# Kernel tuning notes

Hardware: AMD Instinct MI355X
Metric: run time of the kernel (lower is better)

## Reference

```python
import jax, jax.numpy as jnp
import numpy as np

HIDDEN = 32  # hard-coded in the module


def _lstm_cell(x, h, c, W_ih, W_hh, b_ih, b_hh):
    # torch.nn.LSTMCell: gates in order i, f, g, o
    gates = x @ W_ih.T + b_ih + h @ W_hh.T + b_hh
    i, f, g, o = jnp.split(gates, 4, axis=-1)
    c_new = jax.nn.sigmoid(f) * c + jax.nn.sigmoid(i) * jnp.tanh(g)
    h_new = jax.nn.sigmoid(o) * jnp.tanh(c_new)
    return h_new, c_new


def setup_inputs() -> dict:
    key = jax.random.key(0)
    ks = jax.random.split(key, 11)
    B, T, d, len_out = 256, 1024, 8, 10
    s = 0.05
    return {
        "input": jax.random.normal(ks[0], (B, T, d), dtype=jnp.float32),
        "W_ih1": jax.random.normal(ks[1], (4 * HIDDEN, d), dtype=jnp.float32) * s,
        "W_hh1": jax.random.normal(ks[2], (4 * HIDDEN, HIDDEN), dtype=jnp.float32) * s,
        "b_ih1": jax.random.normal(ks[3], (4 * HIDDEN,), dtype=jnp.float32) * s,
        "b_hh1": jax.random.normal(ks[4], (4 * HIDDEN,), dtype=jnp.float32) * s,
        "W_ih2": jax.random.normal(ks[5], (4 * HIDDEN, HIDDEN), dtype=jnp.float32) * s,
        "W_hh2": jax.random.normal(ks[6], (4 * HIDDEN, HIDDEN), dtype=jnp.float32) * s,
        "b_ih2": jax.random.normal(ks[7], (4 * HIDDEN,), dtype=jnp.float32) * s,
        "b_hh2": jax.random.normal(ks[8], (4 * HIDDEN,), dtype=jnp.float32) * s,
        "W_lin": jax.random.normal(ks[9], (d * len_out, HIDDEN), dtype=jnp.float32) * s,
        "b_lin": jax.random.normal(ks[10], (d * len_out,), dtype=jnp.float32) * s,
    }


def reference(input, W_ih1, W_hh1, b_ih1, b_hh1, W_ih2, W_hh2, b_ih2, b_hh2, W_lin, b_lin):
    B, T, d = input.shape
    len_out = W_lin.shape[0] // d

    def step(carry, x_t):
        h1, c1, h2, c2 = carry
        h1, c1 = _lstm_cell(x_t, h1, c1, W_ih1, W_hh1, b_ih1, b_hh1)
        h2, c2 = _lstm_cell(h1, h2, c2, W_ih2, W_hh2, b_ih2, b_hh2)
        out = h2 @ W_lin.T + b_lin  # [B, d*len_out]
        return (h1, c1, h2, c2), out

    z = jnp.zeros((B, HIDDEN), dtype=input.dtype)
    init = (z, z, z, z)
    xs = jnp.swapaxes(input, 0, 1)  # [T, B, d]
    _, outs = jax.lax.scan(step, init, xs)  # [T, B, d*len_out]
    outs = jnp.swapaxes(outs, 0, 1)  # [B, T, d*len_out]
    return outs.reshape(B, T, d, len_out)
```

## Files before the change

kernel.cpp:

```cpp
#include <hip/hip_runtime.h>

#define TT  1024
#define DIN 8

__device__ __forceinline__ float fsig(float x) {
    float e = __builtin_amdgcn_exp2f(-1.4426950408889634f * x);
    return __builtin_amdgcn_rcpf(1.0f + e);
}
__device__ __forceinline__ float ftanh_(float x) {
    float e = __builtin_amdgcn_exp2f(-2.8853900817779268f * x);
    return 2.0f * __builtin_amdgcn_rcpf(1.0f + e) - 1.0f;
}
template<int CTRL>
__device__ __forceinline__ float dppf(float v) {
    return __uint_as_float((unsigned)__builtin_amdgcn_update_dpp(
        0, (int)__float_as_uint(v), CTRL, 0xF, 0xF, true));
}
#define RED8(a)  { a += dppf<0x141>(a); a += dppf<0x1B>(a); a += dppf<0xB1>(a); }

__device__ __forceinline__ void bar_lgkm() {
    asm volatile("s_waitcnt lgkmcnt(0)\n\ts_barrier" ::: "memory");
}

__global__ void __launch_bounds__(512, 2)
lstm_rec(const float* __restrict__ x,
         const float* __restrict__ Wih1, const float* __restrict__ Whh1,
         const float* __restrict__ bih1, const float* __restrict__ bhh1,
         const float* __restrict__ Wih2, const float* __restrict__ Whh2,
         const float* __restrict__ bih2, const float* __restrict__ bhh2,
         float* __restrict__ out)
{
    const int tid = threadIdx.x;
    const int wv  = tid >> 6;
    const int l   = tid & 63;
    const int s   = l & 7;
    const int gi  = l >> 3;
    const int b   = blockIdx.x;
    const bool isL1 = (wv < 4);
    const int  wu   = isL1 ? wv : (wv - 4);
    const int  unit = wu*8 + gi;

    __shared__ float hb1[2][32];
    __shared__ float hb2[2][32];
    if (tid < 64)       ((float*)hb1)[tid]      = 0.f;
    else if (tid < 128) ((float*)hb2)[tid - 64] = 0.f;

    float w[32];
    float bi, bf, bg, bo;
    if (isL1) {
#pragma unroll
        for (int r = 0; r < 4; ++r) {
            const int R = r*32 + unit;
#pragma unroll
            for (int j = 0; j < 4; ++j) w[r*4 + j] = Whh1[R*32 + s*4 + j];
            w[16 + r] = Wih1[R*DIN + s];
        }
        bi = bih1[unit]      + bhh1[unit];
        bf = bih1[32 + unit] + bhh1[32 + unit];
        bg = bih1[64 + unit] + bhh1[64 + unit];
        bo = bih1[96 + unit] + bhh1[96 + unit];
    } else {
        const float* Wb = (s < 4) ? Whh2 : Wih2;
        const int co = (s & 3) * 8;
#pragma unroll
        for (int r = 0; r < 4; ++r) {
            const int R = r*32 + unit;
#pragma unroll
            for (int j = 0; j < 8; ++j) w[r*8 + j] = Wb[R*32 + co + j];
        }
        bi = bih2[unit]      + bhh2[unit];
        bf = bih2[32 + unit] + bhh2[32 + unit];
        bg = bih2[64 + unit] + bhh2[64 + unit];
        bo = bih2[96 + unit] + bhh2[96 + unit];
    }

    float c = 0.f;

    const float* __restrict__ xb = x   + (size_t)b * (TT*DIN);
    float* __restrict__ outb     = out + (size_t)b * (TT*80);

    float xcur = 0.f;
    if (isL1) xcur = xb[s];
    int xoff = DIN + s;
    const int XMAX = (TT-1)*DIN + s;
    int o2 = 0;

    bar_lgkm();

#pragma unroll 1
    for (int t = 0; t <= TT; ++t) {
        const int p0  = t & 1;
        const int pm1 = p0 ^ 1;

        if (isL1) {
            if (t < TT) {
                float4 h4 = *reinterpret_cast<const float4*>(&hb1[pm1][s*4]);
                float ai = w[0] *h4.x + w[16]*xcur;
                float af = w[4] *h4.x + w[17]*xcur;
                float ag = w[8] *h4.x + w[18]*xcur;
                float ao = w[12]*h4.x + w[19]*xcur;
                ai += w[1]*h4.y;  af += w[5]*h4.y;  ag += w[9] *h4.y;  ao += w[13]*h4.y;
                ai += w[2]*h4.z;  af += w[6]*h4.z;  ag += w[10]*h4.z;  ao += w[14]*h4.z;
                ai += w[3]*h4.w;  af += w[7]*h4.w;  ag += w[11]*h4.w;  ao += w[15]*h4.w;
                xcur = xb[xoff];
                xoff = (xoff + DIN > XMAX) ? XMAX : (xoff + DIN);
                RED8(ai); RED8(af); RED8(ag); RED8(ao);
                float si = fsig(ai + bi);
                float sf = fsig(af + bf);
                float tg = ftanh_(ag + bg);
                float so = fsig(ao + bo);
                c = sf * c + si * tg;
                float hv = so * ftanh_(c);
                if (s == 0) hb1[p0][unit] = hv;
            }
        } else {
            if (t >= 1) {
                const float* hin = (s < 4) ? &hb2[p0][(s & 3) * 8]
                                           : &hb1[pm1][(s & 3) * 8];
                float4 u0 = reinterpret_cast<const float4*>(hin)[0];
                float4 u1 = reinterpret_cast<const float4*>(hin)[1];
                float ai = w[0] *u0.x, af = w[8] *u0.x, ag = w[16]*u0.x, ao = w[24]*u0.x;
                ai += w[1]*u0.y;  af += w[9] *u0.y;  ag += w[17]*u0.y;  ao += w[25]*u0.y;
                ai += w[2]*u0.z;  af += w[10]*u0.z;  ag += w[18]*u0.z;  ao += w[26]*u0.z;
                ai += w[3]*u0.w;  af += w[11]*u0.w;  ag += w[19]*u0.w;  ao += w[27]*u0.w;
                ai += w[4]*u1.x;  af += w[12]*u1.x;  ag += w[20]*u1.x;  ao += w[28]*u1.x;
                ai += w[5]*u1.y;  af += w[13]*u1.y;  ag += w[21]*u1.y;  ao += w[29]*u1.y;
                ai += w[6]*u1.z;  af += w[14]*u1.z;  ag += w[22]*u1.z;  ao += w[30]*u1.z;
                ai += w[7]*u1.w;  af += w[15]*u1.w;  ag += w[23]*u1.w;  ao += w[31]*u1.w;
                RED8(ai); RED8(af); RED8(ag); RED8(ao);
                float si = fsig(ai + bi);
                float sf = fsig(af + bf);
                float tg = ftanh_(ag + bg);
                float so = fsig(ao + bo);
                c = sf * c + si * tg;
                float hv = so * ftanh_(c);
                if (s == 0) {
                    hb2[pm1][unit] = hv;
                    outb[o2 + unit] = hv;
                }
                o2 += 80;
            }
        }

        bar_lgkm();
    }
}

__global__ void __launch_bounds__(256, 4)
out_lin(const float* __restrict__ Wlin, const float* __restrict__ blin,
        float* __restrict__ out, int ntiles)
{
    __shared__ float wl[80][36];
    __shared__ float bl[80];
    __shared__ float ht[16][36];
    const int tid = threadIdx.x;

#pragma unroll 1
    for (int i = tid; i < 640; i += 256) {
        const int cc = i >> 3, qq = i & 7;
        float4 v = reinterpret_cast<const float4*>(Wlin)[i];
        *reinterpret_cast<float4*>(&wl[cc][qq*4]) = v;
    }
    if (tid < 80) bl[tid] = blin[tid];
    __syncthreads();

    const int row = tid >> 4;
    const int cl  = tid & 15;

#pragma unroll 1
    for (int tile = blockIdx.x; tile < ntiles; tile += gridDim.x) {
        const size_t base = (size_t)tile * 16;
        if (tid < 128) {
            const int r = tid >> 3, qq = tid & 7;
            float4 v = *reinterpret_cast<const float4*>(out + (base + r)*80 + qq*4);
            *reinterpret_cast<float4*>(&ht[r][qq*4]) = v;
        }
        __syncthreads();

        float hr[32];
#pragma unroll
        for (int j = 0; j < 8; ++j) {
            float4 v = *reinterpret_cast<const float4*>(&ht[row][j*4]);
            hr[4*j]=v.x; hr[4*j+1]=v.y; hr[4*j+2]=v.z; hr[4*j+3]=v.w;
        }
        float res[5];
#pragma unroll
        for (int cj = 0; cj < 5; ++cj) {
            const int cc = cl + 16*cj;
            float a0 = bl[cc], a1 = 0.f, a2 = 0.f, a3 = 0.f;
#pragma unroll
            for (int k = 0; k < 32; k += 4) {
                a0 += wl[cc][k]  *hr[k];   a1 += wl[cc][k+1]*hr[k+1];
                a2 += wl[cc][k+2]*hr[k+2]; a3 += wl[cc][k+3]*hr[k+3];
            }
            res[cj] = (a0 + a1) + (a2 + a3);
        }
        __syncthreads();
#pragma unroll
        for (int cj = 0; cj < 5; ++cj)
            out[(base + row)*80 + cl + 16*cj] = res[cj];
    }
}

extern "C" void kernel_launch(void* const* d_in, const int* in_sizes, int n_in,
                              void* d_out, int out_size, void* d_ws, size_t ws_size,
                              hipStream_t stream) {
    const float* x    = (const float*)d_in[0];
    const float* Wih1 = (const float*)d_in[1];
    const float* Whh1 = (const float*)d_in[2];
    const float* bih1 = (const float*)d_in[3];
    const float* bhh1 = (const float*)d_in[4];
    const float* Wih2 = (const float*)d_in[5];
    const float* Whh2 = (const float*)d_in[6];
    const float* bih2 = (const float*)d_in[7];
    const float* bhh2 = (const float*)d_in[8];
    const float* Wlin = (const float*)d_in[9];
    const float* blin = (const float*)d_in[10];

    const int B = in_sizes[0] / (TT * DIN);
    const int ntiles = (B * TT) / 16;

    hipLaunchKernelGGL(lstm_rec, dim3(B), dim3(512), 0, stream,
                       x, Wih1, Whh1, bih1, bhh1,
                       Wih2, Whh2, bih2, bhh2,
                       (float*)d_out);
    hipLaunchKernelGGL(out_lin, dim3(2048), dim3(256), 0, stream,
                       Wlin, blin, (float*)d_out, ntiles);
}
```

Measured before the change: 425.0 us.

## Split LSTM gates across lanes with 1024-thread blocks and DPP gate exchange

Doubles the recurrent block to 1024 threads so each lane group of 4 computes one gate row instead of 8 lanes computing all four gates. This cuts the per-step dot-product chain, reduction depth and transcendental count per lane: one sigmoid per lane, with tanh for the g gate folded into it. Gate values are then exchanged through row DPP shuffles. In exchange the block barrier now spans 16 waves, and occupancy or register limits change with the new launch bounds.

```diff
diff --git a/kernel.cpp b/kernel.cpp
--- a/kernel.cpp
+++ b/kernel.cpp
@@ -16,13 +16,13 @@
     return __uint_as_float((unsigned)__builtin_amdgcn_update_dpp(
         0, (int)__float_as_uint(v), CTRL, 0xF, 0xF, true));
 }
-#define RED8(a)  { a += dppf<0x141>(a); a += dppf<0x1B>(a); a += dppf<0xB1>(a); }
+#define RED4(a)  { a += dppf<0x1B>(a); a += dppf<0xB1>(a); }
 
 __device__ __forceinline__ void bar_lgkm() {
     asm volatile("s_waitcnt lgkmcnt(0)\n\ts_barrier" ::: "memory");
 }
 
-__global__ void __launch_bounds__(512, 2)
+__global__ void __launch_bounds__(1024, 4)
 lstm_rec(const float* __restrict__ x,
          const float* __restrict__ Wih1, const float* __restrict__ Whh1,
          const float* __restrict__ bih1, const float* __restrict__ bhh1,
@@ -30,48 +30,39 @@
          const float* __restrict__ bih2, const float* __restrict__ bhh2,
          float* __restrict__ out)
 {
-    const int tid = threadIdx.x;
-    const int wv  = tid >> 6;
-    const int l   = tid & 63;
-    const int s   = l & 7;
-    const int gi  = l >> 3;
-    const int b   = blockIdx.x;
-    const bool isL1 = (wv < 4);
-    const int  wu   = isL1 ? wv : (wv - 4);
-    const int  unit = wu*8 + gi;
+    const int tid  = threadIdx.x;
+    const int wv   = tid >> 6;
+    const int l    = tid & 63;
+    const int sl   = l & 3;
+    const int gate = (l >> 2) & 3;
+    const int ul   = l >> 4;
+    const int b    = blockIdx.x;
+    const bool isL1 = (wv < 8);
+    const int  wu   = isL1 ? wv : (wv - 8);
+    const int  unit = wu*4 + ul;
+    const int  R    = gate*32 + unit;
+    const bool isg  = (gate == 2);
 
     __shared__ float hb1[2][32];
     __shared__ float hb2[2][32];
     if (tid < 64)       ((float*)hb1)[tid]      = 0.f;
     else if (tid < 128) ((float*)hb2)[tid - 64] = 0.f;
 
-    float w[32];
-    float bi, bf, bg, bo;
+    float wh[16];
+    float wx0 = 0.f, wx1 = 0.f;
+    float bias;
     if (isL1) {
 #pragma unroll
-        for (int r = 0; r < 4; ++r) {
-            const int R = r*32 + unit;
-#pragma unroll
-            for (int j = 0; j < 4; ++j) w[r*4 + j] = Whh1[R*32 + s*4 + j];
-            w[16 + r] = Wih1[R*DIN + s];
-        }
-        bi = bih1[unit]      + bhh1[unit];
-        bf = bih1[32 + unit] + bhh1[32 + unit];
-        bg = bih1[64 + unit] + bhh1[64 + unit];
-        bo = bih1[96 + unit] + bhh1[96 + unit];
+        for (int j = 0; j < 8; ++j) wh[j] = Whh1[R*32 + sl*8 + j];
+        wx0 = Wih1[R*DIN + sl*2];
+        wx1 = Wih1[R*DIN + sl*2 + 1];
+        bias = bih1[R] + bhh1[R];
     } else {
-        const float* Wb = (s < 4) ? Whh2 : Wih2;
-        const int co = (s & 3) * 8;
-#pragma unroll
-        for (int r = 0; r < 4; ++r) {
-            const int R = r*32 + unit;
-#pragma unroll
-            for (int j = 0; j < 8; ++j) w[r*8 + j] = Wb[R*32 + co + j];
-        }
-        bi = bih2[unit]      + bhh2[unit];
-        bf = bih2[32 + unit] + bhh2[32 + unit];
-        bg = bih2[64 + unit] + bhh2[64 + unit];
-        bo = bih2[96 + unit] + bhh2[96 + unit];
+        const float* Wb = (sl < 2) ? (Whh2 + R*32 + sl*16)
+                                   : (Wih2 + R*32 + (sl-2)*16);
+#pragma unroll
+        for (int j = 0; j < 16; ++j) wh[j] = Wb[j];
+        bias = bih2[R] + bhh2[R];
     }
 
     float c = 0.f;
@@ -79,10 +70,10 @@
     const float* __restrict__ xb = x   + (size_t)b * (TT*DIN);
     float* __restrict__ outb     = out + (size_t)b * (TT*80);
 
-    float xcur = 0.f;
-    if (isL1) xcur = xb[s];
-    int xoff = DIN + s;
-    const int XMAX = (TT-1)*DIN + s;
+    float2 xcur = make_float2(0.f, 0.f);
+    if (isL1) xcur = *reinterpret_cast<const float2*>(xb + sl*2);
+    int xoff = DIN + sl*2;
+    const int XMAX = (TT-1)*DIN + sl*2;
     int o2 = 0;
 
     bar_lgkm();
@@ -94,47 +85,60 @@
 
         if (isL1) {
             if (t < TT) {
-                float4 h4 = *reinterpret_cast<const float4*>(&hb1[pm1][s*4]);
-                float ai = w[0] *h4.x + w[16]*xcur;
-                float af = w[4] *h4.x + w[17]*xcur;
-                float ag = w[8] *h4.x + w[18]*xcur;
-                float ao = w[12]*h4.x + w[19]*xcur;
-                ai += w[1]*h4.y;  af += w[5]*h4.y;  ag += w[9] *h4.y;  ao += w[13]*h4.y;
-                ai += w[2]*h4.z;  af += w[6]*h4.z;  ag += w[10]*h4.z;  ao += w[14]*h4.z;
-                ai += w[3]*h4.w;  af += w[7]*h4.w;  ag += w[11]*h4.w;  ao += w[15]*h4.w;
-                xcur = xb[xoff];
+                const float* hin = &hb1[pm1][sl*8];
+                float4 u0 = reinterpret_cast<const float4*>(hin)[0];
+                float4 u1 = reinterpret_cast<const float4*>(hin)[1];
+                float a0 = wh[0]*u0.x + wx0*xcur.x;
+                float a1 = wh[1]*u0.y + wx1*xcur.y;
+                float a2 = wh[2]*u0.z;
+                float a3 = wh[3]*u0.w;
+                a0 += wh[4]*u1.x;  a1 += wh[5]*u1.y;
+                a2 += wh[6]*u1.z;  a3 += wh[7]*u1.w;
+                xcur = *reinterpret_cast<const float2*>(xb + xoff);
                 xoff = (xoff + DIN > XMAX) ? XMAX : (xoff + DIN);
-                RED8(ai); RED8(af); RED8(ag); RED8(ao);
-                float si = fsig(ai + bi);
-                float sf = fsig(af + bf);
-                float tg = ftanh_(ag + bg);
-                float so = fsig(ao + bo);
-                c = sf * c + si * tg;
+
+                float acc = (a0 + a1) + (a2 + a3);
+                RED4(acc);
+                float full = acc + bias;
+                float u  = isg ? (full + full) : full;
+                float S  = fsig(u);
+                float av = isg ? (S + S - 1.0f) : S;
+                float si = dppf<0x118>(av);
+                float sf = dppf<0x114>(av);
+                float so = dppf<0x104>(av);
+                c = sf * c + si * av;
                 float hv = so * ftanh_(c);
-                if (s == 0) hb1[p0][unit] = hv;
+                if ((l & 15) == 8) hb1[p0][unit] = hv;
             }
         } else {
             if (t >= 1) {
-                const float* hin = (s < 4) ? &hb2[p0][(s & 3) * 8]
-                                           : &hb1[pm1][(s & 3) * 8];
+                const float* hin = (sl < 2) ? &hb2[p0][sl*16]
+                                            : &hb1[pm1][(sl-2)*16];
                 float4 u0 = reinterpret_cast<const float4*>(hin)[0];
                 float4 u1 = reinterpret_cast<const float4*>(hin)[1];
-                float ai = w[0] *u0.x, af = w[8] *u0.x, ag = w[16]*u0.x, ao = w[24]*u0.x;
-                ai += w[1]*u0.y;  af += w[9] *u0.y;  ag += w[17]*u0.y;  ao += w[25]*u0.y;
-                ai += w[2]*u0.z;  af += w[10]*u0.z;  ag += w[18]*u0.z;  ao += w[26]*u0.z;
-                ai += w[3]*u0.w;  af += w[11]*u0.w;  ag += w[19]*u0.w;  ao += w[27]*u0.w;
-                ai += w[4]*u1.x;  af += w[12]*u1.x;  ag += w[20]*u1.x;  ao += w[28]*u1.x;
-                ai += w[5]*u1.y;  af += w[13]*u1.y;  ag += w[21]*u1.y;  ao += w[29]*u1.y;
-                ai += w[6]*u1.z;  af += w[14]*u1.z;  ag += w[22]*u1.z;  ao += w[30]*u1.z;
-                ai += w[7]*u1.w;  af += w[15]*u1.w;  ag += w[23]*u1.w;  ao += w[31]*u1.w;
-                RED8(ai); RED8(af); RED8(ag); RED8(ao);
-                float si = fsig(ai + bi);
-                float sf = fsig(af + bf);
-                float tg = ftanh_(ag + bg);
-                float so = fsig(ao + bo);
-                c = sf * c + si * tg;
+                float4 u2 = reinterpret_cast<const float4*>(hin)[2];
+                float4 u3 = reinterpret_cast<const float4*>(hin)[3];
+                float a0 = wh[0] *u0.x, a1 = wh[1] *u0.y;
+                float a2 = wh[2] *u0.z, a3 = wh[3] *u0.w;
+                a0 += wh[4] *u1.x;  a1 += wh[5] *u1.y;
+                a2 += wh[6] *u1.z;  a3 += wh[7] *u1.w;
+                a0 += wh[8] *u2.x;  a1 += wh[9] *u2.y;
+                a2 += wh[10]*u2.z;  a3 += wh[11]*u2.w;
+                a0 += wh[12]*u3.x;  a1 += wh[13]*u3.y;
+                a2 += wh[14]*u3.z;  a3 += wh[15]*u3.w;
+
+                float acc = (a0 + a1) + (a2 + a3);
+                RED4(acc);
+                float full = acc + bias;
+                float u  = isg ? (full + full) : full;
+                float S  = fsig(u);
+                float av = isg ? (S + S - 1.0f) : S;
+                float si = dppf<0x118>(av);
+                float sf = dppf<0x114>(av);
+                float so = dppf<0x104>(av);
+                c = sf * c + si * av;
                 float hv = so * ftanh_(c);
-                if (s == 0) {
+                if ((l & 15) == 8) {
                     hb2[pm1][unit] = hv;
                     outb[o2 + unit] = hv;
                 }
@@ -220,7 +224,7 @@
     const int B = in_sizes[0] / (TT * DIN);
     const int ntiles = (B * TT) / 16;
 
-    hipLaunchKernelGGL(lstm_rec, dim3(B), dim3(512), 0, stream,
+    hipLaunchKernelGGL(lstm_rec, dim3(B), dim3(1024), 0, stream,
                        x, Wih1, Whh1, bih1, bhh1,
                        Wih2, Whh2, bih2, bhh2,
                        (float*)d_out);
```

Measured after the change: 461.1 us. 8.5% more time.

## Decouple LSTM layers into producer/consumer waves with LDS ring and flags

Applied to the files above, without the earlier changes.

Replaces the 512-thread block with per-timestep barriers by two single-wave roles: wave 0 runs layer 1 and writes h1 into a 256-entry LDS ring, and wave 1 runs layer 2 and consumes the ring. The two waves coordinate through spin-waited progress counters in shared memory instead of block barriers. Each lane pair owns one hidden unit with full-row weights in registers, so packed FMAs and a single DPP swap replace the 8-lane reduction. This removes per-step barrier latency and lets layer 1 run ahead of layer 2. In exchange each wave does more serial work per step, and ordering depends on volatile LDS flags with sleep-based polling.

```diff
diff --git a/kernel.cpp b/kernel.cpp
--- a/kernel.cpp
+++ b/kernel.cpp
@@ -1,7 +1,10 @@
 #include <hip/hip_runtime.h>
 
-#define TT  1024
-#define DIN 8
+#define TT   1024
+#define DIN  8
+#define RING 256
+
+typedef float f32x2 __attribute__((ext_vector_type(2)));
 
 __device__ __forceinline__ float fsig(float x) {
     float e = __builtin_amdgcn_exp2f(-1.4426950408889634f * x);
@@ -16,13 +19,11 @@
     return __uint_as_float((unsigned)__builtin_amdgcn_update_dpp(
         0, (int)__float_as_uint(v), CTRL, 0xF, 0xF, true));
 }
-#define RED8(a)  { a += dppf<0x141>(a); a += dppf<0x1B>(a); a += dppf<0xB1>(a); }
-
-__device__ __forceinline__ void bar_lgkm() {
-    asm volatile("s_waitcnt lgkmcnt(0)\n\ts_barrier" ::: "memory");
-}
-
-__global__ void __launch_bounds__(512, 2)
+__device__ __forceinline__ f32x2 pkfma(f32x2 a, f32x2 b, f32x2 c) {
+    return __builtin_elementwise_fma(a, b, c);
+}
+
+__global__ void __launch_bounds__(128, 1)
 lstm_rec(const float* __restrict__ x,
          const float* __restrict__ Wih1, const float* __restrict__ Whh1,
          const float* __restrict__ bih1, const float* __restrict__ bhh1,
@@ -33,116 +34,150 @@
     const int tid = threadIdx.x;
     const int wv  = tid >> 6;
     const int l   = tid & 63;
-    const int s   = l & 7;
-    const int gi  = l >> 3;
+    const int q   = l & 1;
+    const int j   = l >> 1;
     const int b   = blockIdx.x;
-    const bool isL1 = (wv < 4);
-    const int  wu   = isL1 ? wv : (wv - 4);
-    const int  unit = wu*8 + gi;
-
-    __shared__ float hb1[2][32];
-    __shared__ float hb2[2][32];
-    if (tid < 64)       ((float*)hb1)[tid]      = 0.f;
-    else if (tid < 128) ((float*)hb2)[tid - 64] = 0.f;
-
-    float w[32];
-    float bi, bf, bg, bo;
-    if (isL1) {
-#pragma unroll
-        for (int r = 0; r < 4; ++r) {
-            const int R = r*32 + unit;
-#pragma unroll
-            for (int j = 0; j < 4; ++j) w[r*4 + j] = Whh1[R*32 + s*4 + j];
-            w[16 + r] = Wih1[R*DIN + s];
-        }
-        bi = bih1[unit]      + bhh1[unit];
-        bf = bih1[32 + unit] + bhh1[32 + unit];
-        bg = bih1[64 + unit] + bhh1[64 + unit];
-        bo = bih1[96 + unit] + bhh1[96 + unit];
+    const int r0  = q ? (32 + j) : j;
+    const int r1  = q ? (96 + j) : (64 + j);
+
+    __shared__ float ring[RING][32];
+    __shared__ float hs[2][32];
+    __shared__ int   prog[2];
+    if (tid < 64) ((float*)hs)[tid] = 0.f;
+    if (tid < 2)  prog[tid] = 0;
+    __syncthreads();
+
+    volatile int* vp0 = &prog[0];
+    volatile int* vp1 = &prog[1];
+
+    if (wv == 0) {
+        f32x2 wh0[16], wh1[16], wx0[4], wx1[4];
+#pragma unroll
+        for (int k = 0; k < 16; ++k) {
+            wh0[k] = reinterpret_cast<const f32x2*>(Whh1 + r0*32)[k];
+            wh1[k] = reinterpret_cast<const f32x2*>(Whh1 + r1*32)[k];
+        }
+#pragma unroll
+        for (int k = 0; k < 4; ++k) {
+            wx0[k] = reinterpret_cast<const f32x2*>(Wih1 + r0*DIN)[k];
+            wx1[k] = reinterpret_cast<const f32x2*>(Wih1 + r1*DIN)[k];
+        }
+        const float b0 = bih1[r0] + bhh1[r0];
+        const float b1 = bih1[r1] + bhh1[r1];
+        float c1 = 0.f;
+        const float* __restrict__ xb = x + (size_t)b * (TT*DIN);
+        float4 xa = reinterpret_cast<const float4*>(xb)[0];
+        float4 xc = reinterpret_cast<const float4*>(xb)[1];
+        int xoff = DIN;
+        int w1seen = 0;
+
+#pragma unroll 1
+        for (int t = 0; t < TT; ++t) {
+            if (t - w1seen >= RING - 16) {
+                do { __builtin_amdgcn_s_sleep(2); w1seen = *vp1; }
+                while (t - w1seen >= RING - 16);
+            }
+            asm volatile("" ::: "memory");
+
+            f32x2 a0 = {b0, 0.f}, a1 = {0.f, 0.f};
+            f32x2 g0 = {b1, 0.f}, g1 = {0.f, 0.f};
+#pragma unroll
+            for (int qq = 0; qq < 8; ++qq) {
+                float4 v = reinterpret_cast<const float4*>(&hs[0][0])[qq];
+                f32x2 lo = {v.x, v.y}, hi = {v.z, v.w};
+                a0 = pkfma(wh0[2*qq],   lo, a0);
+                a1 = pkfma(wh0[2*qq+1], hi, a1);
+                g0 = pkfma(wh1[2*qq],   lo, g0);
+                g1 = pkfma(wh1[2*qq+1], hi, g1);
+            }
+            f32x2 xp0 = {xa.x, xa.y}, xp1 = {xa.z, xa.w};
+            f32x2 xp2 = {xc.x, xc.y}, xp3 = {xc.z, xc.w};
+            a0 = pkfma(wx0[0], xp0, a0);  a1 = pkfma(wx0[1], xp1, a1);
+            a0 = pkfma(wx0[2], xp2, a0);  a1 = pkfma(wx0[3], xp3, a1);
+            g0 = pkfma(wx1[0], xp0, g0);  g1 = pkfma(wx1[1], xp1, g1);
+            g0 = pkfma(wx1[2], xp2, g0);  g1 = pkfma(wx1[3], xp3, g1);
+            xa = reinterpret_cast<const float4*>(xb + xoff)[0];
+            xc = reinterpret_cast<const float4*>(xb + xoff)[1];
+            xoff = (xoff + DIN > (TT-1)*DIN) ? (TT-1)*DIN : (xoff + DIN);
+
+            float p0 = (a0.x + a0.y) + (a1.x + a1.y);
+            float p1 = (g0.x + g0.y) + (g1.x + g1.y);
+            float A  = fsig(p0);
+            float uu = q ? p1 : (p1 + p1);
+            float S  = fsig(uu);
+            float Bv = q ? S : (S + S - 1.0f);
+            float An = dppf<0xB1>(A), Bn = dppf<0xB1>(Bv);
+            float si = q ? An : A,  sf = q ? A  : An;
+            float tg = q ? Bn : Bv, so = q ? Bv : Bn;
+            c1 = sf * c1 + si * tg;
+            float h1v = so * ftanh_(c1);
+            if (!q) { hs[0][j] = h1v; ring[t & (RING-1)][j] = h1v; }
+            asm volatile("s_waitcnt lgkmcnt(0)" ::: "memory");
+            if (l == 0) *vp0 = t + 1;
+        }
     } else {
-        const float* Wb = (s < 4) ? Whh2 : Wih2;
-        const int co = (s & 3) * 8;
-#pragma unroll
-        for (int r = 0; r < 4; ++r) {
-            const int R = r*32 + unit;
-#pragma unroll
-            for (int j = 0; j < 8; ++j) w[r*8 + j] = Wb[R*32 + co + j];
-        }
-        bi = bih2[unit]      + bhh2[unit];
-        bf = bih2[32 + unit] + bhh2[32 + unit];
-        bg = bih2[64 + unit] + bhh2[64 + unit];
-        bo = bih2[96 + unit] + bhh2[96 + unit];
-    }
-
-    float c = 0.f;
-
-    const float* __restrict__ xb = x   + (size_t)b * (TT*DIN);
-    float* __restrict__ outb     = out + (size_t)b * (TT*80);
-
-    float xcur = 0.f;
-    if (isL1) xcur = xb[s];
-    int xoff = DIN + s;
-    const int XMAX = (TT-1)*DIN + s;
-    int o2 = 0;
-
-    bar_lgkm();
-
-#pragma unroll 1
-    for (int t = 0; t <= TT; ++t) {
-        const int p0  = t & 1;
-        const int pm1 = p0 ^ 1;
-
-        if (isL1) {
-            if (t < TT) {
-                float4 h4 = *reinterpret_cast<const float4*>(&hb1[pm1][s*4]);
-                float ai = w[0] *h4.x + w[16]*xcur;
-                float af = w[4] *h4.x + w[17]*xcur;
-                float ag = w[8] *h4.x + w[18]*xcur;
-                float ao = w[12]*h4.x + w[19]*xcur;
-                ai += w[1]*h4.y;  af += w[5]*h4.y;  ag += w[9] *h4.y;  ao += w[13]*h4.y;
-                ai += w[2]*h4.z;  af += w[6]*h4.z;  ag += w[10]*h4.z;  ao += w[14]*h4.z;
-                ai += w[3]*h4.w;  af += w[7]*h4.w;  ag += w[11]*h4.w;  ao += w[15]*h4.w;
-                xcur = xb[xoff];
-                xoff = (xoff + DIN > XMAX) ? XMAX : (xoff + DIN);
-                RED8(ai); RED8(af); RED8(ag); RED8(ao);
-                float si = fsig(ai + bi);
-                float sf = fsig(af + bf);
-                float tg = ftanh_(ag + bg);
-                float so = fsig(ao + bo);
-                c = sf * c + si * tg;
-                float hv = so * ftanh_(c);
-                if (s == 0) hb1[p0][unit] = hv;
-            }
-        } else {
-            if (t >= 1) {
-                const float* hin = (s < 4) ? &hb2[p0][(s & 3) * 8]
-                                           : &hb1[pm1][(s & 3) * 8];
-                float4 u0 = reinterpret_cast<const float4*>(hin)[0];
-                float4 u1 = reinterpret_cast<const float4*>(hin)[1];
-                float ai = w[0] *u0.x, af = w[8] *u0.x, ag = w[16]*u0.x, ao = w[24]*u0.x;
-                ai += w[1]*u0.y;  af += w[9] *u0.y;  ag += w[17]*u0.y;  ao += w[25]*u0.y;
-                ai += w[2]*u0.z;  af += w[10]*u0.z;  ag += w[18]*u0.z;  ao += w[26]*u0.z;
-                ai += w[3]*u0.w;  af += w[11]*u0.w;  ag += w[19]*u0.w;  ao += w[27]*u0.w;
-                ai += w[4]*u1.x;  af += w[12]*u1.x;  ag += w[20]*u1.x;  ao += w[28]*u1.x;
-                ai += w[5]*u1.y;  af += w[13]*u1.y;  ag += w[21]*u1.y;  ao += w[29]*u1.y;
-                ai += w[6]*u1.z;  af += w[14]*u1.z;  ag += w[22]*u1.z;  ao += w[30]*u1.z;
-                ai += w[7]*u1.w;  af += w[15]*u1.w;  ag += w[23]*u1.w;  ao += w[31]*u1.w;
-                RED8(ai); RED8(af); RED8(ag); RED8(ao);
-                float si = fsig(ai + bi);
-                float sf = fsig(af + bf);
-                float tg = ftanh_(ag + bg);
-                float so = fsig(ao + bo);
-                c = sf * c + si * tg;
-                float hv = so * ftanh_(c);
-                if (s == 0) {
-                    hb2[pm1][unit] = hv;
-                    outb[o2 + unit] = hv;
-                }
-                o2 += 80;
-            }
-        }
-
-        bar_lgkm();
+        f32x2 u0w[16], u1w[16], v0w[16], v1w[16];
+#pragma unroll
+        for (int k = 0; k < 16; ++k) {
+            u0w[k] = reinterpret_cast<const f32x2*>(Whh2 + r0*32)[k];
+            u1w[k] = reinterpret_cast<const f32x2*>(Whh2 + r1*32)[k];
+            v0w[k] = reinterpret_cast<const f32x2*>(Wih2 + r0*32)[k];
+            v1w[k] = reinterpret_cast<const f32x2*>(Wih2 + r1*32)[k];
+        }
+        const float b0 = bih2[r0] + bhh2[r0];
+        const float b1 = bih2[r1] + bhh2[r1];
+        float c2 = 0.f;
+        float* __restrict__ outb = out + (size_t)b * (TT*80);
+        int o2 = 0;
+        int w0seen = 0;
+
+#pragma unroll 1
+        for (int t = 0; t < TT; ++t) {
+            if (w0seen < t + 1) {
+                do { __builtin_amdgcn_s_sleep(1); w0seen = *vp0; }
+                while (w0seen < t + 1);
+            }
+            asm volatile("" ::: "memory");
+
+            f32x2 a0 = {b0, 0.f}, a1 = {0.f, 0.f};
+            f32x2 g0 = {b1, 0.f}, g1 = {0.f, 0.f};
+            const float* rp = &ring[t & (RING-1)][0];
+#pragma unroll
+            for (int qq = 0; qq < 8; ++qq) {
+                float4 v = reinterpret_cast<const float4*>(rp)[qq];
+                f32x2 lo = {v.x, v.y}, hi = {v.z, v.w};
+                a0 = pkfma(v0w[2*qq],   lo, a0);
+                a1 = pkfma(v0w[2*qq+1], hi, a1);
+                g0 = pkfma(v1w[2*qq],   lo, g0);
+                g1 = pkfma(v1w[2*qq+1], hi, g1);
+            }
+#pragma unroll
+            for (int qq = 0; qq < 8; ++qq) {
+                float4 v = reinterpret_cast<const float4*>(&hs[1][0])[qq];
+                f32x2 lo = {v.x, v.y}, hi = {v.z, v.w};
+                a0 = pkfma(u0w[2*qq],   lo, a0);
+                a1 = pkfma(u0w[2*qq+1], hi, a1);
+                g0 = pkfma(u1w[2*qq],   lo, g0);
+                g1 = pkfma(u1w[2*qq+1], hi, g1);
+            }
+            float p0 = (a0.x + a0.y) + (a1.x + a1.y);
+            float p1 = (g0.x + g0.y) + (g1.x + g1.y);
+            float A  = fsig(p0);
+            float uu = q ? p1 : (p1 + p1);
+            float S  = fsig(uu);
+            float Bv = q ? S : (S + S - 1.0f);
+            float An = dppf<0xB1>(A), Bn = dppf<0xB1>(Bv);
+            float si = q ? An : A,  sf = q ? A  : An;
+            float tg = q ? Bn : Bv, so = q ? Bv : Bn;
+            c2 = sf * c2 + si * tg;
+            float h2v = so * ftanh_(c2);
+            if (!q) { hs[1][j] = h2v; outb[o2 + j] = h2v; }
+            o2 += 80;
+            if ((t & 15) == 15) {
+                asm volatile("s_waitcnt lgkmcnt(0)" ::: "memory");
+                if (l == 0) *vp1 = t + 1;
+            }
+        }
     }
 }
 
@@ -179,9 +214,9 @@
 
         float hr[32];
 #pragma unroll
-        for (int j = 0; j < 8; ++j) {
-            float4 v = *reinterpret_cast<const float4*>(&ht[row][j*4]);
-            hr[4*j]=v.x; hr[4*j+1]=v.y; hr[4*j+2]=v.z; hr[4*j+3]=v.w;
+        for (int jj = 0; jj < 8; ++jj) {
+            float4 v = *reinterpret_cast<const float4*>(&ht[row][jj*4]);
+            hr[4*jj]=v.x; hr[4*jj+1]=v.y; hr[4*jj+2]=v.z; hr[4*jj+3]=v.w;
         }
         float res[5];
 #pragma unroll
@@ -220,7 +255,7 @@
     const int B = in_sizes[0] / (TT * DIN);
     const int ntiles = (B * TT) / 16;
 
-    hipLaunchKernelGGL(lstm_rec, dim3(B), dim3(512), 0, stream,
+    hipLaunchKernelGGL(lstm_rec, dim3(B), dim3(128), 0, stream,
                        x, Wih1, Whh1, bih1, bhh1,
                        Wih2, Whh2, bih2, bhh2,
                        (float*)d_out);
```

Measured after the change: 502.0 us. 18.1% more time.
